# Optimization experiments

Measured on AMD Instinct MI355X. Metric: run time of the kernel, lower is better.

The kernel has to match this reference:

```python
import jax, jax.numpy as jnp
import numpy as np

SEQ = 10; NCH = 7; NNODES = 10; GH = 32; HEADS = 4; LH = 64; NUSERS = 1000

def _edges():
    e = []
    for i in range(4):
        e += [[i, 7], [7, i]]
    for i in range(4, 7):
        e += [[i, 8], [8, i]]
    e += [[7, 8], [8, 7], [7, 9], [9, 7], [8, 9], [9, 8]]
    a = np.array(e, dtype=np.int32)
    return a[:, 0], a[:, 1]

_SRC, _DST = _edges()

def gat_conv(x, W, att_src, att_dst, bias, concat):
    # x: [B,N,Fin], W: [Fin,H,C], att_*: [H,C]. PyG GATConv: adds self-loops, leaky_relu(0.2), edge-softmax by dst.
    src = jnp.concatenate([jnp.asarray(_SRC), jnp.arange(NNODES, dtype=jnp.int32)])
    dst = jnp.concatenate([jnp.asarray(_DST), jnp.arange(NNODES, dtype=jnp.int32)])
    xh = jnp.einsum('bnf,fhc->bnhc', x, W)            # [B,N,H,C]
    a_s = (xh * att_src).sum(-1)                       # [B,N,H]
    a_d = (xh * att_dst).sum(-1)
    e = jax.nn.leaky_relu(a_s[:, src] + a_d[:, dst], 0.2)  # [B,E,H]
    B = x.shape[0]
    m = jnp.full((B, NNODES, e.shape[-1]), -jnp.inf, e.dtype).at[:, dst].max(e)
    p = jnp.exp(e - m[:, dst])
    den = jnp.zeros((B, NNODES, e.shape[-1]), e.dtype).at[:, dst].add(p)
    alpha = p / den[:, dst]                            # softmax over incoming edges
    out = jnp.zeros(xh.shape, xh.dtype).at[:, dst].add(alpha[..., None] * xh[:, src])
    out = out.reshape(B, NNODES, -1) if concat else out.mean(axis=2)
    return out + bias

def graph_conv(x, W_rel, b_rel, W_root):
    # PyG GraphConv(aggr='add'): lin_rel(sum_{j->i} x_j) + lin_root(x_i); no self-loops.
    src = jnp.asarray(_SRC); dst = jnp.asarray(_DST)
    agg = jnp.zeros_like(x).at[:, dst].add(x[:, src])
    return agg @ W_rel + b_rel + x @ W_root

def lstm_dir(x, Wih, Whh, b):
    B, T, _ = x.shape
    H = Whh.shape[1]
    xw = jnp.einsum('btd,gd->btg', x, Wih) + b         # precompute input projections [B,T,4H]
    def step(carry, xt):
        h, c = carry
        g = xt + h @ Whh.T
        i, f, gg, o = jnp.split(g, 4, -1)
        c = jax.nn.sigmoid(f) * c + jax.nn.sigmoid(i) * jnp.tanh(gg)
        h = jax.nn.sigmoid(o) * jnp.tanh(c)
        return (h, c), h
    z = jnp.zeros((B, H), x.dtype)
    _, hs = jax.lax.scan(step, (z, z), xw.transpose(1, 0, 2))
    return hs.transpose(1, 0, 2)

def bilstm(x, Wf, Uf, bf, Wb, Ub, bb):
    fwd = lstm_dir(x, Wf, Uf, bf)
    bwd = lstm_dir(x[:, ::-1], Wb, Ub, bb)[:, ::-1]
    return jnp.concatenate([fwd, bwd], -1)

def self_attn(O, Wa, ba):
    Q = jnp.tanh(O @ Wa.T + ba)
    a = jax.nn.softmax(jnp.einsum('bqh,bkh->bqk', Q, O), axis=-1)
    return jnp.einsum('bqk,bkh->bqh', a, O)

_SPECS = {
    'ga1_W': (SEQ, HEADS, GH), 'ga1_as': (HEADS, GH), 'ga1_ad': (HEADS, GH), 'ga1_b': (HEADS * GH,),
    'ga2_W': (HEADS * GH, 1, SEQ), 'ga2_as': (1, SEQ), 'ga2_ad': (1, SEQ), 'ga2_b': (SEQ,),
    'gp1_Wrel': (SEQ, GH), 'gp1_Wroot': (SEQ, GH), 'gp1_b': (GH,),
    'gp2_Wrel': (GH, SEQ), 'gp2_Wroot': (GH, SEQ), 'gp2_b': (SEQ,),
    'l1f_Wih': (4 * LH, 3 * NCH), 'l1f_Whh': (4 * LH, LH), 'l1f_b': (4 * LH,),
    'l1b_Wih': (4 * LH, 3 * NCH), 'l1b_Whh': (4 * LH, LH), 'l1b_b': (4 * LH,),
    'l2f_Wih': (4 * LH, 2 * LH), 'l2f_Whh': (4 * LH, LH), 'l2f_b': (4 * LH,),
    'l2b_Wih': (4 * LH, 2 * LH), 'l2b_Whh': (4 * LH, LH), 'l2b_b': (4 * LH,),
    'a1_Wa': (2 * LH, 2 * LH), 'a1_ba': (2 * LH,),
    'a2_Wa': (2 * LH, 2 * LH), 'a2_ba': (2 * LH,),
    'fc_W': (NUSERS, 2 * LH), 'fc_b': (NUSERS,),
}

def setup_inputs() -> dict:
    key = jax.random.key(0)
    B = 32768
    keys = jax.random.split(key, len(_SPECS) + 1)
    inp = {'M': jax.random.normal(keys[0], (B, NCH, SEQ), dtype=jnp.float32)}
    for k, (name, shp) in zip(keys[1:], _SPECS.items()):
        inp[name] = (jax.random.normal(k, shp, dtype=jnp.float32) * 0.1)
    return inp

def reference(M, ga1_W, ga1_as, ga1_ad, ga1_b, ga2_W, ga2_as, ga2_ad, ga2_b,
              gp1_Wrel, gp1_Wroot, gp1_b, gp2_Wrel, gp2_Wroot, gp2_b,
              l1f_Wih, l1f_Whh, l1f_b, l1b_Wih, l1b_Whh, l1b_b,
              l2f_Wih, l2f_Whh, l2f_b, l2b_Wih, l2b_Whh, l2b_b,
              a1_Wa, a1_ba, a2_Wa, a2_ba, fc_W, fc_b):
    B = M.shape[0]
    pad = jnp.zeros((B, NNODES - NCH, SEQ), M.dtype)
    nf = jnp.concatenate([M, pad], axis=1)             # [B,10,10]
    h = jax.nn.relu(gat_conv(nf, ga1_W, ga1_as, ga1_ad, ga1_b, True))
    Mp = gat_conv(h, ga2_W, ga2_as, ga2_ad, ga2_b, False)[:, :NCH]
    g = jax.nn.relu(graph_conv(nf, gp1_Wrel, gp1_b, gp1_Wroot))
    bfeat = graph_conv(g, gp2_Wrel, gp2_b, gp2_Wroot)[:, :NCH]
    x = jnp.concatenate([M.transpose(0, 2, 1), Mp.transpose(0, 2, 1), bfeat.transpose(0, 2, 1)], axis=2)
    x = bilstm(x, l1f_Wih, l1f_Whh, l1f_b, l1b_Wih, l1b_Whh, l1b_b)
    x = self_attn(x, a1_Wa, a1_ba)
    x = bilstm(x, l2f_Wih, l2f_Whh, l2f_b, l2b_Wih, l2b_Whh, l2b_b)
    x = self_attn(x, a2_Wa, a2_ba)
    x = x.mean(axis=1)
    return x @ fc_W.T + fc_b
```

## Files before the change

kernel.cpp:

```cpp
#include <hip/hip_runtime.h>
#include <hip/hip_bf16.h>
#include <cstdint>


#define NCH 7
#define SEQ 10
#define NN  10

__constant__ int c_src[20] = {0,7,1,7,2,7,3,7,4,8,5,8,6,8,7,8,7,9,8,9};
__constant__ int c_dst[20] = {7,0,7,1,7,2,7,3,8,4,8,5,8,6,8,7,9,7,9,8};
__constant__ int c_in_start[11] = {0,2,4,6,8,10,12,14,21,27,30};
__constant__ int c_in_edge[30] = {1,20, 3,21, 5,22, 7,23, 9,24, 11,25, 13,26,
                                  0,2,4,6,15,17,27,
                                  8,10,12,14,19,28,
                                  16,18,29};
__constant__ int c_gin_start[11] = {0,1,2,3,4,5,6,7,13,18,20};
__constant__ int c_gin_src[20] = {7,7,7,7,8,8,8, 0,1,2,3,8,9, 4,5,6,7,9, 7,8};

__device__ __forceinline__ float fsig(float x){ return 1.f/(1.f + __expf(-x)); }
__device__ __forceinline__ float ftanh(float x){ return 1.f - 2.f/(__expf(2.f*x) + 1.f); }

typedef _Float16 h2v __attribute__((ext_vector_type(2)));
typedef _Float16 f16x4 __attribute__((ext_vector_type(4)));
typedef float    f32x4 __attribute__((ext_vector_type(4)));

#if defined(__has_builtin)
#if __has_builtin(__builtin_amdgcn_fdot2)
#define HAS_FDOT2 1
#endif
#endif

__device__ __forceinline__ float d2(uint32_t a, uint32_t b, float c){
#ifdef HAS_FDOT2
    return __builtin_amdgcn_fdot2(__builtin_bit_cast(h2v, a),
                                  __builtin_bit_cast(h2v, b), c, false);
#else
    union { uint32_t u; _Float16 h[2]; } ua, ub;
    ua.u = a; ub.u = b;
    return c + (float)ua.h[0]*(float)ub.h[0] + (float)ua.h[1]*(float)ub.h[1];
#endif
}

__device__ __forceinline__ f32x4 mfma16(f16x4 a, f16x4 b, f32x4 c){
    return __builtin_amdgcn_mfma_f32_16x16x16f16(a, b, c, 0, 0, 0);
}
__device__ __forceinline__ f16x4 ld4h(const _Float16* p){
    return __builtin_bit_cast(f16x4, *(const uint2*)(p));
}
__device__ __forceinline__ f16x4 ld4hg(const uint32_t* p){
    return __builtin_bit_cast(f16x4, *(const uint2*)(p));
}

#define IH1O 0
#define HH1O 8192
#define IH2O 24576
#define HH2O 57344
#define WA1O 73728
#define WA2O 81920
#define WPK_TOTAL 90112

__global__ __launch_bounds__(256) void prep_kernel(
    const float* __restrict__ w1f, const float* __restrict__ w1b,
    const float* __restrict__ h1f, const float* __restrict__ h1b,
    const float* __restrict__ w2f, const float* __restrict__ w2b,
    const float* __restrict__ h2f, const float* __restrict__ h2b,
    const float* __restrict__ wa1, const float* __restrict__ wa2,
    uint32_t* __restrict__ wpk)
{
    int i = blockIdx.x * 256 + threadIdx.x;
    if (i >= WPK_TOTAL) return;
    float v0, v1;
    if (i < 73728) {
        const float *sa, *sb; int K, NKT, base;
        if (i < 8192)       { base = 0;     NKT = 2; K = 21;  sa = w1f; sb = w1b; }
        else if (i < 24576) { base = 8192;  NKT = 4; K = 64;  sa = h1f; sb = h1b; }
        else if (i < 57344) { base = 24576; NKT = 8; K = 128; sa = w2f; sb = w2b; }
        else                { base = 57344; NKT = 4; K = 64;  sa = h2f; sb = h2b; }
        int local = i - base;
        int dsz = 16 * NKT * 128;
        const float* src = sa;
        if (local >= dsz) { src = sb; local -= dsz; }
        int entry = local >> 7;
        int lane  = (local & 127) >> 1;
        int j     = local & 1;
        int tau = entry / NKT, kt = entry - tau * NKT;
        int row = 16 * tau + (lane & 15);
        int kb  = kt * 16 + 4 * (lane >> 4) + 2 * j;
        v0 = (kb     < K) ? src[row * K + kb]     : 0.f;
        v1 = (kb + 1 < K) ? src[row * K + kb + 1] : 0.f;
    } else {
        int local = i - 73728;
        const float* src = wa1;
        if (local >= 8192) { src = wa2; local -= 8192; }
        int row = local >> 6, p = local & 63;
        int d0 = 2 * p;
        v0 = src[row * 128 + d0];
        v1 = src[row * 128 + d0 + 1];
    }
    union { _Float16 h[2]; uint32_t u; } x;
    x.h[0] = (_Float16)v0; x.h[1] = (_Float16)v1;
    wpk[i] = x.u;
}

__global__ __launch_bounds__(64) void graph_kernel(
    const float* __restrict__ M,
    const float* __restrict__ W1, const float* __restrict__ as1,
    const float* __restrict__ ad1, const float* __restrict__ b1,
    const float* __restrict__ W2, const float* __restrict__ as2,
    const float* __restrict__ ad2, const float* __restrict__ b2,
    const float* __restrict__ gWrel1, const float* __restrict__ gWroot1,
    const float* __restrict__ gb1,
    const float* __restrict__ gWrel2, const float* __restrict__ gWroot2,
    const float* __restrict__ gb2,
    float* __restrict__ xseq)
{
    const int b = blockIdx.x;
    const int tid = threadIdx.x;

    __shared__ float s_nf[10][10];
    __shared__ float s_xh[10][129];
    __shared__ float s_h[10][129];
    __shared__ float s_as[10][4], s_ad[10][4];
    __shared__ float s_al[30][4];
    __shared__ float s_xh2[10][10];
    __shared__ float s_as2[10], s_ad2[10];
    __shared__ float s_al2[30];
    __shared__ float s_mp[10][10];
    __shared__ float s_agg[10][10];
    __shared__ float s_g[10][33];
    __shared__ float s_gagg[10][33];
    __shared__ float s_bf[10][10];

    const float* Mb = M + (size_t)b * 70;
    for (int i = tid; i < 100; i += 64) {
        int n = i / 10, f = i - n * 10;
        s_nf[n][f] = (n < 7) ? Mb[n * 10 + f] : 0.f;
    }
    float wA[10], wB[10];
    #pragma unroll
    for (int f = 0; f < 10; f++) { wA[f] = W1[f*128 + tid]; wB[f] = W1[f*128 + tid + 64]; }
    __syncthreads();

    for (int n = 0; n < 10; n++) {
        float a0 = 0.f, a1 = 0.f;
        #pragma unroll
        for (int f = 0; f < 10; f++) { float x = s_nf[n][f]; a0 += x*wA[f]; a1 += x*wB[f]; }
        s_xh[n][tid] = a0; s_xh[n][tid + 64] = a1;
    }
    __syncthreads();
    if (tid < 40) {
        int n = tid >> 2, h = tid & 3;
        float va = 0.f, vd = 0.f;
        #pragma unroll
        for (int c = 0; c < 32; c++) {
            float x = s_xh[n][h*32 + c];
            va += x * as1[h*32 + c];
            vd += x * ad1[h*32 + c];
        }
        s_as[n][h] = va; s_ad[n][h] = vd;
    }
    __syncthreads();
    for (int i = tid; i < 120; i += 64) {
        int e = i >> 2, h = i & 3;
        int sn = (e < 20) ? c_src[e] : e - 20;
        int dn = (e < 20) ? c_dst[e] : e - 20;
        float v = s_as[sn][h] + s_ad[dn][h];
        s_al[e][h] = (v >= 0.f) ? v : 0.2f * v;
    }
    __syncthreads();
    if (tid < 40) {
        int n = tid >> 2, h = tid & 3;
        int st = c_in_start[n], en = c_in_start[n+1];
        float m = -1e30f;
        for (int j = st; j < en; j++) m = fmaxf(m, s_al[c_in_edge[j]][h]);
        float den = 0.f;
        for (int j = st; j < en; j++) den += __expf(s_al[c_in_edge[j]][h] - m);
        float inv = 1.f / den;
        for (int j = st; j < en; j++) {
            int e = c_in_edge[j];
            s_al[e][h] = __expf(s_al[e][h] - m) * inv;
        }
    }
    __syncthreads();
    for (int i = tid; i < 1280; i += 64) {
        int n = i >> 7, hc = i & 127, h = hc >> 5;
        int st = c_in_start[n], en = c_in_start[n+1];
        float o = b1[hc];
        for (int j = st; j < en; j++) {
            int e = c_in_edge[j];
            int sn = (e < 20) ? c_src[e] : e - 20;
            o += s_al[e][h] * s_xh[sn][hc];
        }
        s_h[n][hc] = fmaxf(o, 0.f);
    }
    __syncthreads();
    for (int i = tid; i < 100; i += 64) {
        int n = i / 10, c = i - (i / 10) * 10;
        float a = 0.f;
        #pragma unroll 16
        for (int f = 0; f < 128; f++) a += s_h[n][f] * W2[f*10 + c];
        s_xh2[n][c] = a;
    }
    __syncthreads();
    if (tid < 20) {
        int n = (tid < 10) ? tid : tid - 10;
        const float* av = (tid < 10) ? as2 : ad2;
        float v = 0.f;
        #pragma unroll
        for (int c = 0; c < 10; c++) v += s_xh2[n][c] * av[c];
        if (tid < 10) s_as2[n] = v; else s_ad2[n] = v;
    }
    __syncthreads();
    if (tid < 30) {
        int e = tid;
        int sn = (e < 20) ? c_src[e] : e - 20;
        int dn = (e < 20) ? c_dst[e] : e - 20;
        float v = s_as2[sn] + s_ad2[dn];
        s_al2[e] = (v >= 0.f) ? v : 0.2f * v;
    }
    __syncthreads();
    if (tid < 10) {
        int st = c_in_start[tid], en = c_in_start[tid+1];
        float m = -1e30f;
        for (int j = st; j < en; j++) m = fmaxf(m, s_al2[c_in_edge[j]]);
        float den = 0.f;
        for (int j = st; j < en; j++) den += __expf(s_al2[c_in_edge[j]] - m);
        float inv = 1.f / den;
        for (int j = st; j < en; j++) s_al2[c_in_edge[j]] = __expf(s_al2[c_in_edge[j]] - m) * inv;
    }
    __syncthreads();
    for (int i = tid; i < 100; i += 64) {
        int n = i / 10, c = i - (i / 10) * 10;
        int st = c_in_start[n], en = c_in_start[n+1];
        float o = b2[c];
        for (int j = st; j < en; j++) {
            int e = c_in_edge[j];
            int sn = (e < 20) ? c_src[e] : e - 20;
            o += s_al2[e] * s_xh2[sn][c];
        }
        s_mp[n][c] = o;
    }
    __syncthreads();
    for (int i = tid; i < 100; i += 64) {
        int n = i / 10, f = i - (i / 10) * 10;
        int st = c_gin_start[n], en = c_gin_start[n+1];
        float a = 0.f;
        for (int j = st; j < en; j++) a += s_nf[c_gin_src[j]][f];
        s_agg[n][f] = a;
    }
    __syncthreads();
    for (int i = tid; i < 320; i += 64) {
        int n = i >> 5, c = i & 31;
        float v = gb1[c];
        #pragma unroll
        for (int f = 0; f < 10; f++)
            v += s_agg[n][f] * gWrel1[f*32 + c] + s_nf[n][f] * gWroot1[f*32 + c];
        s_g[n][c] = fmaxf(v, 0.f);
    }
    __syncthreads();
    for (int i = tid; i < 320; i += 64) {
        int n = i >> 5, c = i & 31;
        int st = c_gin_start[n], en = c_gin_start[n+1];
        float a = 0.f;
        for (int j = st; j < en; j++) a += s_g[c_gin_src[j]][c];
        s_gagg[n][c] = a;
    }
    __syncthreads();
    for (int i = tid; i < 100; i += 64) {
        int n = i / 10, c = i - (i / 10) * 10;
        float v = gb2[c];
        #pragma unroll
        for (int f = 0; f < 32; f++)
            v += s_gagg[n][f] * gWrel2[f*10 + c] + s_g[n][f] * gWroot2[f*10 + c];
        s_bf[n][c] = v;
    }
    __syncthreads();
    float* xo = xseq + (size_t)b * 210;
    for (int i = tid; i < 210; i += 64) {
        int t = i / 21, k = i - (i / 21) * 21;
        float v;
        if (k < 7)       v = s_nf[k][t];
        else if (k < 14) v = s_mp[k - 7][t];
        else             v = s_bf[k - 14][t];
        xo[i] = v;
    }
}


template<int L>
__device__ __forceinline__ void rec_layer(
    const uint32_t* __restrict__ wpk,
    const float* __restrict__ bf, const float* __restrict__ bb,
    uint32_t* __restrict__ sR1, uint32_t* __restrict__ sO2,
    uint32_t* __restrict__ sH, int w, int l)
{
    constexpr int NKT = (L == 1) ? 2 : 8;
    const uint32_t* bih = wpk + ((L == 1) ? IH1O : IH2O);
    const uint32_t* bhh = wpk + ((L == 1) ? HH1O : HH2O);
    const int dir = w >> 1;
    const int ub  = (w & 1) * 2;
    bih += dir * 16 * NKT * 128;
    bhh += dir * 16 * 4 * 128;
    const float* bias = dir ? bb : bf;
    const int ln = l & 15, lg = l >> 4;
    const int arow = l & 7, asub = 4 * lg;
    float bv[2][4];
    #pragma unroll
    for (int up = 0; up < 2; ++up)
        #pragma unroll
        for (int g = 0; g < 4; ++g)
            bv[up][g] = bias[64 * g + 16 * (ub + up) + ln];
    float cs[2][4] = {{0.f,0.f,0.f,0.f},{0.f,0.f,0.f,0.f}};
    const _Float16* Axh = (const _Float16*)sR1;
    _Float16* Hh  = (_Float16*)sH;
    _Float16* O2h = (_Float16*)sO2;
    for (int ss = 0; ss < 10; ++ss) {
        const int t = dir ? 9 - ss : ss;
        const int cur = ss & 1;
        f16x4 ax[NKT];
        #pragma unroll
        for (int kt = 0; kt < NKT; ++kt) {
            const int fo = (L == 1) ? (arow * 360 + t * 36 + kt * 16 + asub)
                                    : (arow * 1360 + t * 136 + kt * 16 + asub);
            ax[kt] = ld4h(Axh + fo);
        }
        f16x4 ah[4];
        #pragma unroll
        for (int kt = 0; kt < 4; ++kt)
            ah[kt] = ld4h(Hh + ((dir * 2 + cur) * 8 + arow) * 72 + kt * 16 + asub);
        #pragma unroll
        for (int up = 0; up < 2; ++up) {
            const int v = ub + up;
            f32x4 G[4];
            #pragma unroll
            for (int g = 0; g < 4; ++g) {
                const int tau = 4 * g + v;
                f32x4 c = { bv[up][g], bv[up][g], bv[up][g], bv[up][g] };
                #pragma unroll
                for (int kt = 0; kt < NKT; ++kt)
                    c = mfma16(ax[kt], ld4hg(bih + (tau * NKT + kt) * 128 + 2 * l), c);
                #pragma unroll
                for (int kt = 0; kt < 4; ++kt)
                    c = mfma16(ah[kt], ld4hg(bhh + (tau * 4 + kt) * 128 + 2 * l), c);
                G[g] = c;
            }
            if (l < 32) {
                #pragma unroll
                for (int r = 0; r < 4; ++r) {
                    const int s = asub + r;
                    const float ig = fsig(G[0][r]), fg = fsig(G[1][r]);
                    const float gg = ftanh(G[2][r]), og = fsig(G[3][r]);
                    const float c2 = fg * cs[up][r] + ig * gg;
                    cs[up][r] = c2;
                    const float hv = og * ftanh(c2);
                    const int u = 16 * v + ln;
                    Hh[((dir * 2 + (1 - cur)) * 8 + s) * 72 + u] = (_Float16)hv;
                    O2h[s * 1360 + t * 136 + dir * 64 + u] = (_Float16)hv;
                }
            }
        }
        __syncthreads();
    }
}

__device__ __forceinline__ void attn_one(
    const uint32_t* __restrict__ wa, const float* __restrict__ ba,
    uint32_t* __restrict__ sR1, const uint32_t* __restrict__ sO2,
    float* __restrict__ sSC, int l, int s, float* __restrict__ outg)
{
    const uint32_t* O2s = sO2 + s * 680;
    uint32_t* Q2s = sR1 + s * 680;
    float* sc = sSC + s * 104;

    float qa0[10], qa1[10];
    {
        float b0 = ba[l], b1 = ba[64 + l];
        #pragma unroll
        for (int t = 0; t < 10; t++) { qa0[t] = b0; qa1[t] = b1; }
    }
    #pragma unroll 4
    for (int c = 0; c < 16; c++) {
        uint4 w0 = *(const uint4*)(wa + l * 64 + c * 4);
        uint4 w1 = *(const uint4*)(wa + (64 + l) * 64 + c * 4);
        #pragma unroll
        for (int t = 0; t < 10; t++) {
            uint4 o = *(const uint4*)(O2s + t * 68 + c * 4);
            qa0[t] = d2(w0.w, o.w, d2(w0.z, o.z, d2(w0.y, o.y, d2(w0.x, o.x, qa0[t]))));
            qa1[t] = d2(w1.w, o.w, d2(w1.z, o.z, d2(w1.y, o.y, d2(w1.x, o.x, qa1[t]))));
        }
    }
    _Float16* q2h = (_Float16*)Q2s;
    #pragma unroll
    for (int t = 0; t < 10; t++) {
        q2h[t * 136 + l]      = (_Float16)ftanh(qa0[t]);
        q2h[t * 136 + 64 + l] = (_Float16)ftanh(qa1[t]);
    }
    #pragma unroll
    for (int r = 0; r < 2; r++) {
        int idx = l + r * 64;
        if (idx < 100) {
            int q = idx / 10, k = idx - 10 * q;
            float sv = 0.f;
            #pragma unroll
            for (int m = 0; m < 16; m++) {
                uint4 a = *(const uint4*)(Q2s + q * 68 + m * 4);
                uint4 b = *(const uint4*)(O2s + k * 68 + m * 4);
                sv = d2(a.w, b.w, d2(a.z, b.z, d2(a.y, b.y, d2(a.x, b.x, sv))));
            }
            sc[idx] = sv;
        }
    }
    if (l < 10) {
        float m = -1e30f;
        #pragma unroll
        for (int k = 0; k < 10; k++) m = fmaxf(m, sc[l * 10 + k]);
        float den = 0.f, e[10];
        #pragma unroll
        for (int k = 0; k < 10; k++) { e[k] = __expf(sc[l * 10 + k] - m); den += e[k]; }
        float inv = 1.f / den;
        #pragma unroll
        for (int k = 0; k < 10; k++) sc[l * 10 + k] = e[k] * inv;
    }
    float of0[10], of1[10];
    {
        const _Float16* o2h = (const _Float16*)O2s;
        #pragma unroll
        for (int k = 0; k < 10; k++) {
            of0[k] = (float)o2h[k * 136 + l];
            of1[k] = (float)o2h[k * 136 + 64 + l];
        }
    }
    float pa0[10], pa1[10];
    #pragma unroll
    for (int t = 0; t < 10; t++) { pa0[t] = 0.f; pa1[t] = 0.f; }
    #pragma unroll
    for (int k = 0; k < 10; k++) {
        float o0 = of0[k], o1 = of1[k];
        #pragma unroll
        for (int t = 0; t < 10; t++) {
            float sv = sc[t * 10 + k];
            pa0[t] += sv * o0; pa1[t] += sv * o1;
        }
    }
    if (outg) {
        float s0 = 0.f, s1 = 0.f;
        #pragma unroll
        for (int t = 0; t < 10; t++) { s0 += pa0[t]; s1 += pa1[t]; }
        outg[l] = s0 * 0.1f; outg[64 + l] = s1 * 0.1f;
    } else {
        _Float16* a2h = (_Float16*)Q2s;
        #pragma unroll
        for (int t = 0; t < 10; t++) {
            a2h[t * 136 + l]      = (_Float16)pa0[t];
            a2h[t * 136 + 64 + l] = (_Float16)pa1[t];
        }
    }
}

__global__ __launch_bounds__(256) void seq_kernel(
    const float* __restrict__ xseq, const uint32_t* __restrict__ wpk,
    const float* __restrict__ b1f, const float* __restrict__ b1b,
    const float* __restrict__ b2f, const float* __restrict__ b2b,
    const float* __restrict__ ba1, const float* __restrict__ ba2,
    float* __restrict__ xbar)
{
    __shared__ __align__(16) uint32_t sR1[8 * 680];
    __shared__ __align__(16) uint32_t sO2[8 * 680];
    __shared__ __align__(16) float    sSC[8 * 104];
    __shared__ __align__(16) uint32_t sH[1152];
    const int tid = threadIdx.x;
    const int w = tid >> 6, l = tid & 63;
    const int b0 = blockIdx.x * 8;

    {
        _Float16* xh = (_Float16*)sR1;
        const float* xs = xseq + (size_t)b0 * 210;
        for (int i = tid; i < 2880; i += 256) {
            int s = i / 360, r = i - s * 360;
            int t = r / 36, k = r - t * 36;
            float v = (k < 21) ? xs[s * 210 + t * 21 + k] : 0.f;
            xh[s * 360 + t * 36 + k] = (_Float16)v;
        }
    }
    for (int i = tid; i < 1152; i += 256) sH[i] = 0;
    __syncthreads();

    rec_layer<1>(wpk, b1f, b1b, sR1, sO2, sH, w, l);

    for (int smp = 0; smp < 2; ++smp)
        attn_one(wpk + WA1O, ba1, sR1, sO2, sSC, l, 2 * w + smp, nullptr);
    __syncthreads();
    for (int i = tid; i < 1152; i += 256) sH[i] = 0;
    __syncthreads();

    rec_layer<2>(wpk, b2f, b2b, sR1, sO2, sH, w, l);

    for (int smp = 0; smp < 2; ++smp) {
        int s = 2 * w + smp;
        attn_one(wpk + WA2O, ba2, sR1, sO2, sSC, l, s,
                 xbar + (size_t)(b0 + s) * 128);
    }
}

__global__ __launch_bounds__(256) void fc_kernel(
    const float* __restrict__ xbar, const float* __restrict__ W,
    const float* __restrict__ fb, float* __restrict__ out, int B)
{
    __shared__ __align__(16) float s_xb[64 * 132];
    const int tid = threadIdx.x;
    const int b0 = blockIdx.y * 64;
    const int u0 = blockIdx.x * 64;

    for (int i = tid; i < 64 * 128; i += 256) {
        int s = i >> 7, k = i & 127;
        int bb = b0 + s;
        s_xb[s * 132 + k] = (bb < B) ? xbar[(size_t)bb * 128 + k] : 0.f;
    }
    __syncthreads();

    const int tx = tid & 15, ty = tid >> 4;
    float acc[4][4] = {};
    for (int k = 0; k < 128; k += 4) {
        float4 wv[4], xv[4];
        #pragma unroll
        for (int j = 0; j < 4; j++) {
            int u = u0 + tx + 16 * j;
            int uc = (u < 1000) ? u : 999;
            wv[j] = *(const float4*)(W + (size_t)uc * 128 + k);
        }
        #pragma unroll
        for (int si = 0; si < 4; si++) {
            int s = ty + 16 * si;
            xv[si] = *(const float4*)(s_xb + s * 132 + k);
        }
        #pragma unroll
        for (int j = 0; j < 4; j++)
            #pragma unroll
            for (int si = 0; si < 4; si++)
                acc[j][si] += wv[j].x*xv[si].x + wv[j].y*xv[si].y
                            + wv[j].z*xv[si].z + wv[j].w*xv[si].w;
    }
    #pragma unroll
    for (int j = 0; j < 4; j++) {
        int u = u0 + tx + 16 * j;
        if (u < 1000) {
            float bb = fb[u];
            #pragma unroll
            for (int si = 0; si < 4; si++) {
                int bsm = b0 + ty + 16 * si;
                if (bsm < B) out[(size_t)bsm * 1000 + u] = acc[j][si] + bb;
            }
        }
    }
}

extern "C" void kernel_launch(void* const* d_in, const int* in_sizes, int n_in,
                              void* d_out, int out_size, void* d_ws, size_t ws_size,
                              hipStream_t stream)
{
    const float* M       = (const float*)d_in[0];
    const float* ga1_W   = (const float*)d_in[1];
    const float* ga1_as  = (const float*)d_in[2];
    const float* ga1_ad  = (const float*)d_in[3];
    const float* ga1_b   = (const float*)d_in[4];
    const float* ga2_W   = (const float*)d_in[5];
    const float* ga2_as  = (const float*)d_in[6];
    const float* ga2_ad  = (const float*)d_in[7];
    const float* ga2_b   = (const float*)d_in[8];
    const float* gp1_Wrel  = (const float*)d_in[9];
    const float* gp1_Wroot = (const float*)d_in[10];
    const float* gp1_b     = (const float*)d_in[11];
    const float* gp2_Wrel  = (const float*)d_in[12];
    const float* gp2_Wroot = (const float*)d_in[13];
    const float* gp2_b     = (const float*)d_in[14];
    const float* l1f_Wih = (const float*)d_in[15];
    const float* l1f_Whh = (const float*)d_in[16];
    const float* l1f_b   = (const float*)d_in[17];
    const float* l1b_Wih = (const float*)d_in[18];
    const float* l1b_Whh = (const float*)d_in[19];
    const float* l1b_b   = (const float*)d_in[20];
    const float* l2f_Wih = (const float*)d_in[21];
    const float* l2f_Whh = (const float*)d_in[22];
    const float* l2f_b   = (const float*)d_in[23];
    const float* l2b_Wih = (const float*)d_in[24];
    const float* l2b_Whh = (const float*)d_in[25];
    const float* l2b_b   = (const float*)d_in[26];
    const float* a1_Wa   = (const float*)d_in[27];
    const float* a1_ba   = (const float*)d_in[28];
    const float* a2_Wa   = (const float*)d_in[29];
    const float* a2_ba   = (const float*)d_in[30];
    const float* fc_W    = (const float*)d_in[31];
    const float* fc_b    = (const float*)d_in[32];

    const int B = in_sizes[0] / 70;

    float* xseq = (float*)d_ws;
    float* xbar = (float*)((char*)d_ws + (size_t)B * 210 * 4);
    uint32_t* wpk = (uint32_t*)((char*)d_ws + (size_t)B * 210 * 4
                                            + (size_t)B * 128 * 4);

    prep_kernel<<<(WPK_TOTAL + 255) / 256, 256, 0, stream>>>(
        l1f_Wih, l1b_Wih, l1f_Whh, l1b_Whh,
        l2f_Wih, l2b_Wih, l2f_Whh, l2b_Whh,
        a1_Wa, a2_Wa, wpk);

    graph_kernel<<<B, 64, 0, stream>>>(M,
        ga1_W, ga1_as, ga1_ad, ga1_b,
        ga2_W, ga2_as, ga2_ad, ga2_b,
        gp1_Wrel, gp1_Wroot, gp1_b,
        gp2_Wrel, gp2_Wroot, gp2_b,
        xseq);

    seq_kernel<<<B / 8, 256, 0, stream>>>(xseq, wpk,
        l1f_b, l1b_b, l2f_b, l2b_b, a1_ba, a2_ba, xbar);

    dim3 fgrid((1000 + 63) / 64, (B + 63) / 64);
    fc_kernel<<<fgrid, 256, 0, stream>>>(xbar, fc_W, fc_b, (float*)d_out, B);
}
```

Measured before the change: 2.650 ms.

## Drop block barriers in single-wave graph kernel and pack GAT activations as fp16

Because the graph kernel launches exactly one 64-thread wavefront per block, every __syncthreads is replaced by a compiler scheduling barrier. The code relies on LDS operations from a single wave staying in order. The GAT layer-1 projections, hidden activations and layer-2 weights are now stored as packed fp16 pairs in shared memory. The attention scores and the second projection use fdot2, which halves LDS traffic and instruction count. This trades fp32 precision for fp16 in intermediate GAT activations. The graph kernel is likely a minor part of the total time next to the recurrent layers.

```diff
diff --git a/kernel.cpp b/kernel.cpp
--- a/kernel.cpp
+++ b/kernel.cpp
@@ -50,6 +50,15 @@
 __device__ __forceinline__ f16x4 ld4hg(const uint32_t* p){
     return __builtin_bit_cast(f16x4, *(const uint2*)(p));
 }
+__device__ __forceinline__ uint32_t pk2(float a, float b){
+    union { _Float16 h[2]; uint32_t u; } x;
+    x.h[0] = (_Float16)a; x.h[1] = (_Float16)b; return x.u;
+}
+__device__ __forceinline__ float2 upk2(uint32_t u){
+    union { uint32_t u; _Float16 h[2]; } x; x.u = u;
+    return make_float2((float)x.h[0], (float)x.h[1]);
+}
+#define SBAR() __builtin_amdgcn_sched_barrier(0)
 
 #define IH1O 0
 #define HH1O 8192
@@ -117,9 +126,11 @@
     const int b = blockIdx.x;
     const int tid = threadIdx.x;
 
-    __shared__ float s_nf[10][10];
-    __shared__ float s_xh[10][129];
-    __shared__ float s_h[10][129];
+    __shared__ float    s_nf[10][10];
+    __shared__ uint32_t s_xhp[10][64];
+    __shared__ uint32_t s_hp[10][64];
+    __shared__ uint32_t s_w2p[10][64];
+    __shared__ uint32_t s_a1p[64], s_d1p[64];
     __shared__ float s_as[10][4], s_ad[10][4];
     __shared__ float s_al[30][4];
     __shared__ float s_xh2[10][10];
@@ -136,30 +147,43 @@
         int n = i / 10, f = i - n * 10;
         s_nf[n][f] = (n < 7) ? Mb[n * 10 + f] : 0.f;
     }
-    float wA[10], wB[10];
-    #pragma unroll
-    for (int f = 0; f < 10; f++) { wA[f] = W1[f*128 + tid]; wB[f] = W1[f*128 + tid + 64]; }
-    __syncthreads();
-
+    s_a1p[tid] = pk2(as1[2 * tid], as1[2 * tid + 1]);
+    s_d1p[tid] = pk2(ad1[2 * tid], ad1[2 * tid + 1]);
+    for (int i = tid; i < 640; i += 64) {
+        int c = i >> 6, j = i & 63;
+        s_w2p[c][j] = pk2(W2[(2 * j) * 10 + c], W2[(2 * j + 1) * 10 + c]);
+    }
+    float2 w1r[10];
+    #pragma unroll
+    for (int f = 0; f < 10; f++)
+        w1r[f] = *(const float2*)(W1 + f * 128 + 2 * tid);
+    SBAR();
+
+    #pragma unroll
     for (int n = 0; n < 10; n++) {
         float a0 = 0.f, a1 = 0.f;
         #pragma unroll
-        for (int f = 0; f < 10; f++) { float x = s_nf[n][f]; a0 += x*wA[f]; a1 += x*wB[f]; }
-        s_xh[n][tid] = a0; s_xh[n][tid + 64] = a1;
-    }
-    __syncthreads();
+        for (int f = 0; f < 10; f++) {
+            float x = s_nf[n][f];
+            a0 += x * w1r[f].x; a1 += x * w1r[f].y;
+        }
+        s_xhp[n][tid] = pk2(a0, a1);
+    }
+    SBAR();
+
     if (tid < 40) {
         int n = tid >> 2, h = tid & 3;
         float va = 0.f, vd = 0.f;
         #pragma unroll
-        for (int c = 0; c < 32; c++) {
-            float x = s_xh[n][h*32 + c];
-            va += x * as1[h*32 + c];
-            vd += x * ad1[h*32 + c];
+        for (int cp = 0; cp < 16; cp++) {
+            uint32_t x = s_xhp[n][h * 16 + cp];
+            va = d2(x, s_a1p[h * 16 + cp], va);
+            vd = d2(x, s_d1p[h * 16 + cp], vd);
         }
         s_as[n][h] = va; s_ad[n][h] = vd;
     }
-    __syncthreads();
+    SBAR();
+
     for (int i = tid; i < 120; i += 64) {
         int e = i >> 2, h = i & 3;
         int sn = (e < 20) ? c_src[e] : e - 20;
@@ -167,7 +191,8 @@
         float v = s_as[sn][h] + s_ad[dn][h];
         s_al[e][h] = (v >= 0.f) ? v : 0.2f * v;
     }
-    __syncthreads();
+    SBAR();
+
     if (tid < 40) {
         int n = tid >> 2, h = tid & 3;
         int st = c_in_start[n], en = c_in_start[n+1];
@@ -181,27 +206,35 @@
             s_al[e][h] = __expf(s_al[e][h] - m) * inv;
         }
     }
-    __syncthreads();
-    for (int i = tid; i < 1280; i += 64) {
-        int n = i >> 7, hc = i & 127, h = hc >> 5;
+    SBAR();
+
+    for (int i = tid; i < 640; i += 64) {
+        int n = i >> 6, p = i & 63;
+        int h = p >> 4;
         int st = c_in_start[n], en = c_in_start[n+1];
-        float o = b1[hc];
+        float2 bb = *(const float2*)(b1 + 2 * p);
+        float o0 = bb.x, o1 = bb.y;
         for (int j = st; j < en; j++) {
             int e = c_in_edge[j];
             int sn = (e < 20) ? c_src[e] : e - 20;
-            o += s_al[e][h] * s_xh[sn][hc];
-        }
-        s_h[n][hc] = fmaxf(o, 0.f);
-    }
-    __syncthreads();
+            float al = s_al[e][h];
+            float2 xf = upk2(s_xhp[sn][p]);
+            o0 += al * xf.x; o1 += al * xf.y;
+        }
+        s_hp[n][p] = pk2(fmaxf(o0, 0.f), fmaxf(o1, 0.f));
+    }
+    SBAR();
+
     for (int i = tid; i < 100; i += 64) {
         int n = i / 10, c = i - (i / 10) * 10;
         float a = 0.f;
         #pragma unroll 16
-        for (int f = 0; f < 128; f++) a += s_h[n][f] * W2[f*10 + c];
+        for (int j = 0; j < 64; j++)
+            a = d2(s_hp[n][j], s_w2p[c][j], a);
         s_xh2[n][c] = a;
     }
-    __syncthreads();
+    SBAR();
+
     if (tid < 20) {
         int n = (tid < 10) ? tid : tid - 10;
         const float* av = (tid < 10) ? as2 : ad2;
@@ -210,7 +243,7 @@
         for (int c = 0; c < 10; c++) v += s_xh2[n][c] * av[c];
         if (tid < 10) s_as2[n] = v; else s_ad2[n] = v;
     }
-    __syncthreads();
+    SBAR();
     if (tid < 30) {
         int e = tid;
         int sn = (e < 20) ? c_src[e] : e - 20;
@@ -218,7 +251,7 @@
         float v = s_as2[sn] + s_ad2[dn];
         s_al2[e] = (v >= 0.f) ? v : 0.2f * v;
     }
-    __syncthreads();
+    SBAR();
     if (tid < 10) {
         int st = c_in_start[tid], en = c_in_start[tid+1];
         float m = -1e30f;
@@ -228,7 +261,7 @@
         float inv = 1.f / den;
         for (int j = st; j < en; j++) s_al2[c_in_edge[j]] = __expf(s_al2[c_in_edge[j]] - m) * inv;
     }
-    __syncthreads();
+    SBAR();
     for (int i = tid; i < 100; i += 64) {
         int n = i / 10, c = i - (i / 10) * 10;
         int st = c_in_start[n], en = c_in_start[n+1];
@@ -240,7 +273,8 @@
         }
         s_mp[n][c] = o;
     }
-    __syncthreads();
+    SBAR();
+
     for (int i = tid; i < 100; i += 64) {
         int n = i / 10, f = i - (i / 10) * 10;
         int st = c_gin_start[n], en = c_gin_start[n+1];
@@ -248,7 +282,7 @@
         for (int j = st; j < en; j++) a += s_nf[c_gin_src[j]][f];
         s_agg[n][f] = a;
     }
-    __syncthreads();
+    SBAR();
     for (int i = tid; i < 320; i += 64) {
         int n = i >> 5, c = i & 31;
         float v = gb1[c];
@@ -257,7 +291,7 @@
             v += s_agg[n][f] * gWrel1[f*32 + c] + s_nf[n][f] * gWroot1[f*32 + c];
         s_g[n][c] = fmaxf(v, 0.f);
     }
-    __syncthreads();
+    SBAR();
     for (int i = tid; i < 320; i += 64) {
         int n = i >> 5, c = i & 31;
         int st = c_gin_start[n], en = c_gin_start[n+1];
@@ -265,7 +299,7 @@
         for (int j = st; j < en; j++) a += s_g[c_gin_src[j]][c];
         s_gagg[n][c] = a;
     }
-    __syncthreads();
+    SBAR();
     for (int i = tid; i < 100; i += 64) {
         int n = i / 10, c = i - (i / 10) * 10;
         float v = gb2[c];
@@ -274,7 +308,8 @@
             v += s_gagg[n][f] * gWrel2[f*10 + c] + s_g[n][f] * gWroot2[f*10 + c];
         s_bf[n][c] = v;
     }
-    __syncthreads();
+    SBAR();
+
     float* xo = xseq + (size_t)b * 210;
     for (int i = tid; i < 210; i += 64) {
         int t = i / 21, k = i - (i / 21) * 21;
```

Result: faster. 2.408 ms (-9.1%).
